# Kernel optimization log

Hardware: AMD Instinct MI355X
Metric: run time of the kernel (lower is better)

The kernel has to match this reference:

```python
import jax, jax.numpy as jnp
import numpy as np
import math

D_MODEL = 256
TEMPERATURE = 10000.0
BIN_SIZE = 0.1
SCALE = 2.0 * math.pi
NUM_POS_FEATS = (D_MODEL // 6) - ((D_MODEL // 6) % 2)  # 42
PAD = D_MODEL - NUM_POS_FEATS * 6                       # 4
PAD_LEFT = PAD // 2                                     # 2


def setup_inputs() -> dict:
    key = jax.random.key(0)
    x = jax.random.uniform(key, (16, 8192, 6), dtype=jnp.float32)
    return {"x": x}


def reference(x):
    B, N, _ = x.shape
    xs = x / BIN_SIZE
    dim_t = jnp.arange(NUM_POS_FEATS, dtype=jnp.float32)
    dim_t = TEMPERATURE ** (2.0 * jnp.floor(dim_t / 2.0) / NUM_POS_FEATS)
    # (B, N, 6, F): each of the 6 coords scaled by frequency bands
    pos = xs[:, :, :, None] * SCALE / dim_t
    # even-index freqs go to sin, odd-index freqs to cos, concatenated over the 6 coords
    to_sin = pos[:, :, :, 0::2].transpose(0, 1, 2, 3).reshape(B, N, 6 * (NUM_POS_FEATS // 2))
    to_cos = pos[:, :, :, 1::2].reshape(B, N, 6 * (NUM_POS_FEATS // 2))
    # left zero-pad to d_model//2 (sin(0)=0, cos(0)=1 as in original)
    to_sin = jnp.pad(to_sin, ((0, 0), (0, 0), (PAD_LEFT, 0)))
    to_cos = jnp.pad(to_cos, ((0, 0), (0, 0), (PAD_LEFT, 0)))
    s = jnp.sin(to_sin)  # (B, N, D/2)
    c = jnp.cos(to_cos)  # (B, N, D/2)
    # ones @ block-diag 2x2 rotation sums each column: even col = cos+sin, odd col = cos-sin
    enc = jnp.stack([c + s, c - s], axis=-1).reshape(B, N, D_MODEL)
    return enc
```

## Files before the change

### kernel.cpp

```cpp
#include <hip/hip_runtime.h>


#define TWENTY_PI          62.83185307179586f
#define LOG2_10000_OVER_21 0.6327482085499738f

__global__ __launch_bounds__(256) void pheno_rotary_pe_kernel(
        const float* __restrict__ x,
        float4* __restrict__ out,
        int npos) {
    int idx = blockIdx.x * blockDim.x + threadIdx.x;
    int pos = idx >> 6;
    int t   = idx & 63;
    if (pos >= npos) return;

    const float* xp = x + pos * 6;

    float vals[4];
#pragma unroll
    for (int q = 0; q < 2; ++q) {
        int k = 2 * t + q;
        float even, odd;
        if (k < 2) {
            even = 1.0f;
            odd  = 1.0f;
        } else {
            int j = k - 2;
            int coord = j / 21;
            int f = j - coord * 21;
            float scale = TWENTY_PI *
                __builtin_amdgcn_exp2f(-LOG2_10000_OVER_21 * (float)f);
            float a = xp[coord] * scale;
            float s = __sinf(a);
            float c = __cosf(a);
            even = c + s;
            odd  = c - s;
        }
        vals[2 * q]     = even;
        vals[2 * q + 1] = odd;
    }

    float4 o;
    o.x = vals[0]; o.y = vals[1]; o.z = vals[2]; o.w = vals[3];
    out[idx] = o;
}

extern "C" void kernel_launch(void* const* d_in, const int* in_sizes, int n_in,
                              void* d_out, int out_size, void* d_ws, size_t ws_size,
                              hipStream_t stream) {
    const float* x = (const float*)d_in[0];
    float4* out = (float4*)d_out;

    int npos = in_sizes[0] / 6;
    int nthreads = npos * 64;
    int block = 256;
    int grid = (nthreads + block - 1) / block;

    pheno_rotary_pe_kernel<<<grid, block, 0, stream>>>(x, out, npos);
}
```

Before: 144.7 us.

## Use single phase-shifted hardware sin/cos with shared-memory frequency table

Rewrites cos(a)+sin(a) and cos(a)-sin(a) as sqrt2*sin(r) and sqrt2*cos(r), where r is the angle in revolutions shifted by 1/8 and reduced with fract. The reduced value goes straight into the hardware v_sin/v_cos instructions, which removes the costlier __sinf/__cosf range reduction. Per-column frequency scales and coordinate indices are computed once per block into a shared table instead of per thread, and outputs use nontemporal stores. The change adds a block-level sync and an LDS read, and may shift precision slightly because the hardware trig instructions are approximate.

```diff
diff --git a/kernel.cpp b/kernel.cpp
--- a/kernel.cpp
+++ b/kernel.cpp
@@ -1,54 +1,57 @@
 #include <hip/hip_runtime.h>
 
 
-#define TWENTY_PI          62.83185307179586f
 #define LOG2_10000_OVER_21 0.6327482085499738f
+#define SQRT2              1.4142135623730951f
+
+typedef float v4f __attribute__((ext_vector_type(4)));
 
 __global__ __launch_bounds__(256) void pheno_rotary_pe_kernel(
         const float* __restrict__ x,
-        float4* __restrict__ out,
+        v4f* __restrict__ out,
         int npos) {
-    int idx = blockIdx.x * blockDim.x + threadIdx.x;
+    __shared__ float2 tbl[128];
+
+    int tid = threadIdx.x;
+    if (tid < 128) {
+        float s = 0.0f;
+        int   c = 0;
+        if (tid >= 2) {
+            int j = tid - 2;
+            c = j / 21;
+            int f = j - 21 * c;
+            s = 10.0f * __builtin_amdgcn_exp2f(-LOG2_10000_OVER_21 * (float)f);
+        }
+        tbl[tid] = make_float2(s, __int_as_float(c));
+    }
+    __syncthreads();
+
+    int idx = blockIdx.x * 256 + tid;
     int pos = idx >> 6;
-    int t   = idx & 63;
     if (pos >= npos) return;
 
+    v4f e = ((const v4f*)tbl)[idx & 63];
     const float* xp = x + pos * 6;
 
-    float vals[4];
-#pragma unroll
-    for (int q = 0; q < 2; ++q) {
-        int k = 2 * t + q;
-        float even, odd;
-        if (k < 2) {
-            even = 1.0f;
-            odd  = 1.0f;
-        } else {
-            int j = k - 2;
-            int coord = j / 21;
-            int f = j - coord * 21;
-            float scale = TWENTY_PI *
-                __builtin_amdgcn_exp2f(-LOG2_10000_OVER_21 * (float)f);
-            float a = xp[coord] * scale;
-            float s = __sinf(a);
-            float c = __cosf(a);
-            even = c + s;
-            odd  = c - s;
-        }
-        vals[2 * q]     = even;
-        vals[2 * q + 1] = odd;
-    }
+    float r0 = __builtin_amdgcn_fractf(
+                   fmaf(xp[__float_as_int(e.y)], e.x, 0.125f));
+    float r1 = __builtin_amdgcn_fractf(
+                   fmaf(xp[__float_as_int(e.w)], e.z, 0.125f));
 
-    float4 o;
-    o.x = vals[0]; o.y = vals[1]; o.z = vals[2]; o.w = vals[3];
-    out[idx] = o;
+    v4f o;
+    o.x = SQRT2 * __builtin_amdgcn_sinf(r0);
+    o.y = SQRT2 * __builtin_amdgcn_cosf(r0);
+    o.z = SQRT2 * __builtin_amdgcn_sinf(r1);
+    o.w = SQRT2 * __builtin_amdgcn_cosf(r1);
+
+    __builtin_nontemporal_store(o, &out[idx]);
 }
 
 extern "C" void kernel_launch(void* const* d_in, const int* in_sizes, int n_in,
                               void* d_out, int out_size, void* d_ws, size_t ws_size,
                               hipStream_t stream) {
     const float* x = (const float*)d_in[0];
-    float4* out = (float4*)d_out;
+    v4f* out = (v4f*)d_out;
 
     int npos = in_sizes[0] / 6;
     int nthreads = npos * 64;
```

New measurement: 143.9 us. No clear change (-0.6%).
